# Kernel tuning notes

Hardware: AMD Instinct MI355X
Metric: run time of the kernel (lower is better)

## Reference

```python
import jax, jax.numpy as jnp
import numpy as np

B, S, D, E, H, K = 4, 2048, 1024, 8, 4096, 2


def setup_inputs() -> dict:
    key = jax.random.key(0)
    ks = jax.random.split(key, 6)
    scale_in = 0.02  # keep logits/activations in a sane range
    return {
        "x": jax.random.normal(ks[0], (B, S, D), jnp.float32),
        "gate_w": jax.random.normal(ks[1], (D, E), jnp.float32) * scale_in,
        "noise_weight": jnp.zeros((E,), jnp.float32),  # torch init: zeros
        "noise": jax.random.normal(ks[2], (B, S, E), jnp.float32),
        "w1": jax.random.normal(ks[3], (E, D, H), jnp.float32) * scale_in,
        "b1": jnp.zeros((E, H), jnp.float32),
        "w2": jax.random.normal(ks[4], (E, D, H), jnp.float32) * scale_in,
        "b2": jnp.zeros((E, H), jnp.float32),
        "wp": jax.random.normal(ks[5], (E, H, D), jnp.float32) * scale_in,
        "bp": jnp.zeros((E, D), jnp.float32),
    }


def _moe(x, gate_w, noise_weight, noise, w1, b1, w2, b2, wp, bp):
    b, s, d = x.shape
    # --- noisy top-k gate ---
    logits = jnp.einsum("bsd,de->bse", x, gate_w)          # [B,S,E]
    logits_noisy = logits + noise * noise_weight            # noisy_std = 1.0
    top_v, top_i = jax.lax.top_k(logits_noisy, K)           # [B,S,K]
    # softmax over sparse logits (-inf elsewhere) == softmax over the top-k values
    probs_k = jax.nn.softmax(top_v, axis=-1)                # [B,S,K]
    onehot = jax.nn.one_hot(top_i, E, dtype=x.dtype)        # [B,S,K,E]
    gated = jnp.einsum("bsk,bske->bse", probs_k, onehot)    # [B,S,E]

    # --- dispatch / expert SwiGLU / weighted combine ---
    xf = x.reshape(b * s, d)                                # [T,D]
    gf = gated.reshape(b * s, E).T                          # [E,T]

    def body(acc, p):
        w1e, b1e, w2e, b2e, wpe, bpe, ge = p
        h = (xf @ w1e + b1e) * jax.nn.silu(xf @ w2e + b2e)  # [T,H] SwiGLU
        out = h @ wpe + bpe                                 # [T,D]
        return acc + ge[:, None] * out, None

    acc, _ = jax.lax.scan(body, jnp.zeros_like(xf), (w1, b1, w2, b2, wp, bp, gf))
    return acc.reshape(b, s, d)


def reference(x, gate_w, noise_weight, noise, w1, b1, w2, b2, wp, bp):
    return _moe(x, gate_w, noise_weight, noise, w1, b1, w2, b2, wp, bp)
```

## Files before the change

### kernel.cpp

```cpp
#include <hip/hip_runtime.h>


#define T_TOK 8192
#define DDIM 1024
#define EEXP 8
#define HDIM 4096
#define RMAX 18432

typedef short short8 __attribute__((ext_vector_type(8)));
typedef float f32x4 __attribute__((ext_vector_type(4)));
typedef unsigned short ushort4v __attribute__((ext_vector_type(4)));
typedef unsigned int u32;

__device__ __forceinline__ unsigned short f2bf(float f) {
  unsigned u = __builtin_bit_cast(unsigned, f);
  return (unsigned short)((u + 0x7FFFu + ((u >> 16) & 1u)) >> 16);
}
__device__ __forceinline__ float bf2f(unsigned short b) {
  unsigned u = ((unsigned)b) << 16;
  return __builtin_bit_cast(float, u);
}
__device__ __forceinline__ void gl_lds16(const void* g, void* l) {
  __builtin_amdgcn_global_load_lds((const u32 __attribute__((address_space(1)))*)g,
                                   (u32 __attribute__((address_space(3)))*)l, 16, 0, 0);
}

__global__ void k_convert_w(const float* __restrict__ src, unsigned short* __restrict__ dst,
                            int N, int K) {
  __shared__ float lbuf[64 * 129];
  int e = blockIdx.z, ct = blockIdx.x, kt = blockIdx.y;
  int tid = threadIdx.x;
  const float* s = src + (size_t)e * K * N + (size_t)(kt * 64) * N + ct * 128;
#pragma unroll
  for (int q = 0; q < 8; q++) {
    int idx = q * 256 + tid;
    int row = idx >> 5, c4 = (idx & 31) * 4;
    float4 v = *(const float4*)(s + (size_t)row * N + c4);
    lbuf[row * 129 + c4 + 0] = v.x;
    lbuf[row * 129 + c4 + 1] = v.y;
    lbuf[row * 129 + c4 + 2] = v.z;
    lbuf[row * 129 + c4 + 3] = v.w;
  }
  __syncthreads();
  unsigned short* dt = dst + ((size_t)(e * (N / 128) + ct) * (K / 64) + kt) * 8192;
#pragma unroll
  for (int q = 0; q < 4; q++) {
    int idx = q * 256 + tid;
    int kc = idx & 7, n = idx >> 3;
    short8 o;
#pragma unroll
    for (int j = 0; j < 8; j++) o[j] = (short)f2bf(lbuf[(kc * 8 + j) * 129 + n]);
    int byte = (n * 128 + kc * 16) ^ ((n & 7) << 4);
    *(short8*)((char*)dt + byte) = o;
  }
}

__global__ void k_init(int* __restrict__ rowtok, int* __restrict__ counts, int* __restrict__ cursor) {
  int i = blockIdx.x * 256 + threadIdx.x;
  if (i < RMAX) rowtok[i] = 0;
  if (i < EEXP) { counts[i] = 0; cursor[i] = 0; }
}

__launch_bounds__(256)
__global__ void k_gate(const float* __restrict__ x, const float* __restrict__ gw,
                       const float* __restrict__ nwt, const float* __restrict__ noi,
                       int* __restrict__ tki, float* __restrict__ tkp,
                       int* __restrict__ counts, unsigned short* __restrict__ xb) {
  __shared__ float gwT[8][1024];
  int tid = threadIdx.x;
#pragma unroll
  for (int q = 0; q < 32; q++) {
    int flat = q * 256 + tid;
    gwT[flat & 7][flat >> 3] = gw[flat];
  }
  __syncthreads();
  int wave = tid >> 6, l = tid & 63;
  int t = blockIdx.x * 4 + wave;
  float acc[8] = {0.f, 0.f, 0.f, 0.f, 0.f, 0.f, 0.f, 0.f};
  const float4* xr = (const float4*)(x + (size_t)t * DDIM);
#pragma unroll
  for (int i = 0; i < 4; i++) {
    float4 xv = xr[l + i * 64];
    int d0 = (l + i * 64) * 4;
    ushort4v o;
    o.x = f2bf(xv.x); o.y = f2bf(xv.y); o.z = f2bf(xv.z); o.w = f2bf(xv.w);
    *(ushort4v*)(xb + (size_t)t * DDIM + d0) = o;
#pragma unroll
    for (int e = 0; e < 8; e++) {
      float4 gv = *(const float4*)&gwT[e][d0];
      acc[e] += xv.x * gv.x + xv.y * gv.y + xv.z * gv.z + xv.w * gv.w;
    }
  }
#pragma unroll
  for (int s = 1; s < 64; s <<= 1) {
#pragma unroll
    for (int e = 0; e < 8; e++) acc[e] += __shfl_xor(acc[e], s, 64);
  }
  if (l == 0) {
    float nl[8];
#pragma unroll
    for (int e = 0; e < 8; e++) nl[e] = acc[e] + noi[t * 8 + e] * nwt[e];
    int i0 = 0; float v0 = nl[0];
#pragma unroll
    for (int e = 1; e < 8; e++) if (nl[e] > v0) { v0 = nl[e]; i0 = e; }
    int i1 = -1; float v1 = -3.4e38f;
#pragma unroll
    for (int e = 0; e < 8; e++) if (e != i0 && nl[e] > v1) { v1 = nl[e]; i1 = e; }
    float ex = __expf(v1 - v0);
    float p0 = 1.f / (1.f + ex);
    float p1 = ex * p0;
    tki[2 * t] = i0; tki[2 * t + 1] = i1;
    tkp[2 * t] = p0; tkp[2 * t + 1] = p1;
    atomicAdd(&counts[i0], 1);
    atomicAdd(&counts[i1], 1);
  }
}

__global__ void k_prefix(const int* __restrict__ counts, int* __restrict__ basep) {
  if (threadIdx.x == 0) {
    int b = 0;
    for (int e = 0; e < EEXP; e++) { basep[e] = b; b += (counts[e] + 255) & ~255; }
  }
}

__global__ void k_scatter(const int* __restrict__ tki, const int* __restrict__ basep,
                          int* __restrict__ cursor, int* __restrict__ rowtok,
                          int* __restrict__ t2r) {
  int t = blockIdx.x * 256 + threadIdx.x;
  if (t >= T_TOK) return;
#pragma unroll
  for (int k = 0; k < 2; k++) {
    int e = tki[2 * t + k];
    int pos = atomicAdd(&cursor[e], 1);
    int row = basep[e] + pos;
    rowtok[row] = t;
    t2r[2 * t + k] = row;
  }
}

__launch_bounds__(512, 2)
__global__ void k_gemm1(const unsigned short* __restrict__ xb,
                        const unsigned short* __restrict__ w1s, const unsigned short* __restrict__ w2s,
                        const float* __restrict__ b1g, const float* __restrict__ b2g,
                        const int* __restrict__ counts, const int* __restrict__ basep,
                        const int* __restrict__ rowtok,
                        unsigned short* __restrict__ hout) {
  int e = blockIdx.y >> 6;
  int rt = blockIdx.y & 63;
  int cnt = counts[e];
  if (rt >= ((cnt + 255) >> 8)) return;
  int ct = blockIdx.x;
  int row0 = basep[e] + rt * 256;
  int col0 = ct * 128;

  __shared__ char smem[131072];
  __shared__ int s_tok[256];
  __shared__ float s_b1[128], s_b2[128];

  int tid = threadIdx.x;
  if (tid < 256) s_tok[tid] = rowtok[row0 + tid];
  if (tid < 128) {
    s_b1[tid] = b1g[e * HDIM + col0 + tid];
    s_b2[tid] = b2g[e * HDIM + col0 + tid];
  }
  __syncthreads();

  int wave = tid >> 6, l = tid & 63;
  int wm = wave >> 2, wn = wave & 3;
  int g = l >> 4, ln = l & 15;

  size_t a_src[4]; int a_dst[4];
#pragma unroll
  for (int q = 0; q < 4; q++) {
    int c = q * 512 + tid;
    int r = c >> 3, cc = (c & 7) ^ (r & 7);
    a_src[q] = (size_t)s_tok[r] * (DDIM * 2) + cc * 16;
    a_dst[q] = c * 16;
  }

  f32x4 zero = {0.f, 0.f, 0.f, 0.f};
  f32x4 acc_a[8][2], acc_b[8][2];
#pragma unroll
  for (int m = 0; m < 8; m++)
#pragma unroll
    for (int n = 0; n < 2; n++) { acc_a[m][n] = zero; acc_b[m][n] = zero; }

  const char* xbb = (const char*)xb;
  const char* w1t = (const char*)(w1s + ((size_t)(e * 32 + ct) * 16) * 8192);
  const char* w2t = (const char*)(w2s + ((size_t)(e * 32 + ct) * 16) * 8192);

#define STAGE1(buf, kt)                                                          \
  {                                                                              \
    int _kt = (kt);                                                              \
    _Pragma("unroll") for (int q = 0; q < 4; q++)                                \
      gl_lds16(xbb + a_src[q] + _kt * 128, smem + (buf) * 32768 + a_dst[q]);     \
    _Pragma("unroll") for (int q = 0; q < 2; q++) {                              \
      int c = q * 512 + tid;                                                     \
      gl_lds16(w1t + (size_t)_kt * 16384 + c * 16, smem + 65536 + (buf) * 16384 + c * 16); \
      gl_lds16(w2t + (size_t)_kt * 16384 + c * 16, smem + 98304 + (buf) * 16384 + c * 16); \
    }                                                                            \
  }

  STAGE1(0, 0);
  __syncthreads();

  int cur = 0;
  for (int kt = 0; kt < 16; kt++) {
    if (kt < 15) STAGE1(cur ^ 1, kt + 1);
#pragma unroll
    for (int ks = 0; ks < 2; ks++) {
      int kb = ks * 64 + g * 16;
      short8 af[8], bf1[2], bf2[2];
#pragma unroll
      for (int m = 0; m < 8; m++) {
        int r = wm * 128 + m * 16 + ln;
        af[m] = *(const short8*)(smem + cur * 32768 + ((r * 128 + kb) ^ ((r & 7) << 4)));
      }
#pragma unroll
      for (int n = 0; n < 2; n++) {
        int r = wn * 32 + n * 16 + ln;
        int byte = (r * 128 + kb) ^ ((r & 7) << 4);
        bf1[n] = *(const short8*)(smem + 65536 + cur * 16384 + byte);
        bf2[n] = *(const short8*)(smem + 98304 + cur * 16384 + byte);
      }
#pragma unroll
      for (int m = 0; m < 8; m++)
#pragma unroll
        for (int n = 0; n < 2; n++) {
          acc_a[m][n] = __builtin_amdgcn_mfma_f32_16x16x32_bf16(af[m], bf1[n], acc_a[m][n], 0, 0, 0);
          acc_b[m][n] = __builtin_amdgcn_mfma_f32_16x16x32_bf16(af[m], bf2[n], acc_b[m][n], 0, 0, 0);
        }
    }
    __syncthreads();
    cur ^= 1;
  }

  unsigned short* ht = (unsigned short*)smem;
#pragma unroll
  for (int m = 0; m < 8; m++)
#pragma unroll
    for (int n = 0; n < 2; n++)
#pragma unroll
      for (int r = 0; r < 4; r++) {
        int row = wm * 128 + m * 16 + g * 4 + r;
        int col = wn * 32 + n * 16 + ln;
        float a = acc_a[m][n][r] + s_b1[col];
        float b = acc_b[m][n][r] + s_b2[col];
        float hv = a * (b / (1.f + __expf(-b)));
        ht[row * 128 + col] = f2bf(hv);
      }
  __syncthreads();
#pragma unroll
  for (int q = 0; q < 8; q++) {
    int idx = q * 512 + tid;
    int row = idx >> 4, cc = (idx & 15) * 8;
    short8 v = *(const short8*)(smem + idx * 16);
    *(short8*)(hout + (size_t)(row0 + row) * HDIM + col0 + cc) = v;
  }
}

__launch_bounds__(512, 2)
__global__ void k_gemm2(const unsigned short* __restrict__ hin,
                        const unsigned short* __restrict__ wps, const float* __restrict__ bpg,
                        const int* __restrict__ counts, const int* __restrict__ basep,
                        unsigned short* __restrict__ yout) {
  int e = blockIdx.y >> 6;
  int rt = blockIdx.y & 63;
  int cnt = counts[e];
  if (rt >= ((cnt + 127) >> 7)) return;
  int ct = blockIdx.x;
  int row0 = basep[e] + rt * 128;
  int col0 = ct * 256;

  __shared__ char smem[98304];
  __shared__ float s_bp[256];
  int tid = threadIdx.x;
  if (tid < 256) s_bp[tid] = bpg[e * DDIM + col0 + tid];
  __syncthreads();

  int wave = tid >> 6, l = tid & 63;
  int wm = wave >> 2, wn = wave & 3;
  int g = l >> 4, ln = l & 15;

  size_t a_src[2]; int a_dst[2];
#pragma unroll
  for (int q = 0; q < 2; q++) {
    int c = q * 512 + tid;
    int r = c >> 3, cc = (c & 7) ^ (r & 7);
    a_src[q] = (size_t)(row0 + r) * (HDIM * 2) + cc * 16;
    a_dst[q] = c * 16;
  }

  f32x4 zero = {0.f, 0.f, 0.f, 0.f};
  f32x4 acc[4][4];
#pragma unroll
  for (int m = 0; m < 4; m++)
#pragma unroll
    for (int n = 0; n < 4; n++) acc[m][n] = zero;

  const char* hb = (const char*)hin;
  const char* wpt = (const char*)(wps + ((size_t)(e * 8 + ct * 2) * 64) * 8192);

#define STAGE2(buf, kt)                                                          \
  {                                                                              \
    int _kt = (kt);                                                              \
    _Pragma("unroll") for (int q = 0; q < 2; q++)                                \
      gl_lds16(hb + a_src[q] + _kt * 128, smem + (buf) * 16384 + a_dst[q]);      \
    _Pragma("unroll") for (int q = 0; q < 4; q++) {                              \
      int c = q * 512 + tid;                                                     \
      int sub = c >> 10;                                                         \
      gl_lds16(wpt + (size_t)(sub * 64 + _kt) * 16384 + (c & 1023) * 16,         \
               smem + 32768 + (buf) * 32768 + c * 16);                           \
    }                                                                            \
  }

  STAGE2(0, 0);
  __syncthreads();

  int cur = 0;
  for (int kt = 0; kt < 64; kt++) {
    if (kt < 63) STAGE2(cur ^ 1, kt + 1);
#pragma unroll
    for (int ks = 0; ks < 2; ks++) {
      int kb = ks * 64 + g * 16;
      short8 af[4], bf[4];
#pragma unroll
      for (int m = 0; m < 4; m++) {
        int r = wm * 64 + m * 16 + ln;
        af[m] = *(const short8*)(smem + cur * 16384 + ((r * 128 + kb) ^ ((r & 7) << 4)));
      }
#pragma unroll
      for (int n = 0; n < 4; n++) {
        int rg = wn * 64 + n * 16 + ln;
        int sub = rg >> 7, rr = rg & 127;
        bf[n] = *(const short8*)(smem + 32768 + cur * 32768 + sub * 16384 +
                                 ((rr * 128 + kb) ^ ((rr & 7) << 4)));
      }
#pragma unroll
      for (int m = 0; m < 4; m++)
#pragma unroll
        for (int n = 0; n < 4; n++)
          acc[m][n] = __builtin_amdgcn_mfma_f32_16x16x32_bf16(af[m], bf[n], acc[m][n], 0, 0, 0);
    }
    __syncthreads();
    cur ^= 1;
  }

  unsigned short* ht = (unsigned short*)smem;
#pragma unroll
  for (int m = 0; m < 4; m++)
#pragma unroll
    for (int n = 0; n < 4; n++)
#pragma unroll
      for (int r = 0; r < 4; r++) {
        int row = wm * 64 + m * 16 + g * 4 + r;
        int col = wn * 64 + n * 16 + ln;
        ht[row * 256 + col] = f2bf(acc[m][n][r] + s_bp[col]);
      }
  __syncthreads();
#pragma unroll
  for (int q = 0; q < 8; q++) {
    int idx = q * 512 + tid;
    int row = idx >> 5, cc = (idx & 31) * 8;
    short8 v = *(const short8*)(smem + idx * 16);
    *(short8*)(yout + (size_t)(row0 + row) * DDIM + col0 + cc) = v;
  }
}

__global__ void k_combine(const unsigned short* __restrict__ yv,
                          const int* __restrict__ t2r, const float* __restrict__ tkp,
                          float* __restrict__ outp) {
  int gid = blockIdx.x * 256 + threadIdx.x;
  int t = gid >> 8;
  int c4 = (gid & 255) << 2;
  int r0 = t2r[2 * t], r1 = t2r[2 * t + 1];
  float p0 = tkp[2 * t], p1 = tkp[2 * t + 1];
  ushort4v u0 = *(const ushort4v*)(yv + (size_t)r0 * DDIM + c4);
  ushort4v u1 = *(const ushort4v*)(yv + (size_t)r1 * DDIM + c4);
  float4 o;
  o.x = p0 * bf2f(u0.x) + p1 * bf2f(u1.x);
  o.y = p0 * bf2f(u0.y) + p1 * bf2f(u1.y);
  o.z = p0 * bf2f(u0.z) + p1 * bf2f(u1.z);
  o.w = p0 * bf2f(u0.w) + p1 * bf2f(u1.w);
  *(float4*)(outp + (size_t)t * DDIM + c4) = o;
}

extern "C" void kernel_launch(void* const* d_in, const int* in_sizes, int n_in,
                              void* d_out, int out_size, void* d_ws, size_t ws_size,
                              hipStream_t stream) {
  const float* x   = (const float*)d_in[0];
  const float* gw  = (const float*)d_in[1];
  const float* nwt = (const float*)d_in[2];
  const float* noi = (const float*)d_in[3];
  const float* w1  = (const float*)d_in[4];
  const float* b1  = (const float*)d_in[5];
  const float* w2  = (const float*)d_in[6];
  const float* b2  = (const float*)d_in[7];
  const float* wp  = (const float*)d_in[8];
  const float* bp  = (const float*)d_in[9];
  float* outp = (float*)d_out;
  char* ws = (char*)d_ws;

  constexpr size_t SZ_W = (size_t)EEXP * DDIM * HDIM * 2;
  constexpr size_t OFF_XB  = 0;
  constexpr size_t OFF_W1S = OFF_XB + (size_t)T_TOK * DDIM * 2;
  constexpr size_t OFF_W2S = OFF_W1S + SZ_W;
  constexpr size_t OFF_WPS = OFF_W2S + SZ_W;
  constexpr size_t OFF_H   = OFF_WPS + SZ_W;
  constexpr size_t OFF_Y   = OFF_H + (size_t)RMAX * HDIM * 2;
  constexpr size_t OFF_RT  = OFF_Y + (size_t)RMAX * DDIM * 2;
  constexpr size_t OFF_TKI = OFF_RT + (size_t)RMAX * 4;
  constexpr size_t OFF_TKP = OFF_TKI + (size_t)T_TOK * 2 * 4;
  constexpr size_t OFF_T2R = OFF_TKP + (size_t)T_TOK * 2 * 4;
  constexpr size_t OFF_CNT = OFF_T2R + (size_t)T_TOK * 2 * 4;
  constexpr size_t OFF_BAS = OFF_CNT + 256;
  constexpr size_t OFF_CUR = OFF_BAS + 256;

  unsigned short* xb  = (unsigned short*)(ws + OFF_XB);
  unsigned short* w1s = (unsigned short*)(ws + OFF_W1S);
  unsigned short* w2s = (unsigned short*)(ws + OFF_W2S);
  unsigned short* wps = (unsigned short*)(ws + OFF_WPS);
  unsigned short* h   = (unsigned short*)(ws + OFF_H);
  unsigned short* y   = (unsigned short*)(ws + OFF_Y);
  int*   rowtok = (int*)(ws + OFF_RT);
  int*   tki    = (int*)(ws + OFF_TKI);
  float* tkp    = (float*)(ws + OFF_TKP);
  int*   t2r    = (int*)(ws + OFF_T2R);
  int*   counts = (int*)(ws + OFF_CNT);
  int*   basep  = (int*)(ws + OFF_BAS);
  int*   cursor = (int*)(ws + OFF_CUR);

  dim3 blk(256);
  k_init<<<dim3((RMAX + 255) / 256), blk, 0, stream>>>(rowtok, counts, cursor);
  k_gate<<<dim3(T_TOK / 4), blk, 0, stream>>>(x, gw, nwt, noi, tki, tkp, counts, xb);
  k_convert_w<<<dim3(HDIM / 128, DDIM / 64, EEXP), blk, 0, stream>>>(w1, w1s, HDIM, DDIM);
  k_convert_w<<<dim3(HDIM / 128, DDIM / 64, EEXP), blk, 0, stream>>>(w2, w2s, HDIM, DDIM);
  k_convert_w<<<dim3(DDIM / 128, HDIM / 64, EEXP), blk, 0, stream>>>(wp, wps, DDIM, HDIM);
  k_prefix<<<dim3(1), dim3(64), 0, stream>>>(counts, basep);
  k_scatter<<<dim3(T_TOK / 256), blk, 0, stream>>>(tki, basep, cursor, rowtok, t2r);
  k_gemm1<<<dim3(HDIM / 128, EEXP * 64), dim3(512), 0, stream>>>(xb, w1s, w2s, b1, b2, counts, basep, rowtok, h);
  k_gemm2<<<dim3(DDIM / 256, EEXP * 64), dim3(512), 0, stream>>>(h, wps, bp, counts, basep, y);
  k_combine<<<dim3(T_TOK), blk, 0, stream>>>(y, t2r, tkp, outp);
  (void)in_sizes; (void)n_in; (void)out_size; (void)ws_size;
}
```

Before: 1.081 ms.

## Deepen GEMM pipelines to 4-stage K=32 slots with split barriers and priority

```diff
diff --git a/kernel.cpp b/kernel.cpp
--- a/kernel.cpp
+++ b/kernel.cpp
@@ -24,34 +24,38 @@
   __builtin_amdgcn_global_load_lds((const u32 __attribute__((address_space(1)))*)g,
                                    (u32 __attribute__((address_space(3)))*)l, 16, 0, 0);
 }
+#define BAR() asm volatile("s_barrier" ::: "memory")
+__device__ __forceinline__ void vwait_c(int n) {
+  if (n == 8) asm volatile("s_waitcnt vmcnt(8)" ::: "memory");
+  else if (n == 4) asm volatile("s_waitcnt vmcnt(4)" ::: "memory");
+  else if (n == 0) asm volatile("s_waitcnt vmcnt(0)" ::: "memory");
+}
+#define MFMA_BF16 __builtin_amdgcn_mfma_f32_16x16x32_bf16
 
 __global__ void k_convert_w(const float* __restrict__ src, unsigned short* __restrict__ dst,
                             int N, int K) {
-  __shared__ float lbuf[64 * 129];
+  __shared__ float lbuf[32][130];
   int e = blockIdx.z, ct = blockIdx.x, kt = blockIdx.y;
   int tid = threadIdx.x;
-  const float* s = src + (size_t)e * K * N + (size_t)(kt * 64) * N + ct * 128;
-#pragma unroll
-  for (int q = 0; q < 8; q++) {
+  const float* s = src + (size_t)e * K * N + (size_t)(kt * 32) * N + ct * 128;
+#pragma unroll
+  for (int q = 0; q < 4; q++) {
     int idx = q * 256 + tid;
     int row = idx >> 5, c4 = (idx & 31) * 4;
     float4 v = *(const float4*)(s + (size_t)row * N + c4);
-    lbuf[row * 129 + c4 + 0] = v.x;
-    lbuf[row * 129 + c4 + 1] = v.y;
-    lbuf[row * 129 + c4 + 2] = v.z;
-    lbuf[row * 129 + c4 + 3] = v.w;
-  }
-  __syncthreads();
-  unsigned short* dt = dst + ((size_t)(e * (N / 128) + ct) * (K / 64) + kt) * 8192;
-#pragma unroll
-  for (int q = 0; q < 4; q++) {
+    lbuf[row][c4 + 0] = v.x; lbuf[row][c4 + 1] = v.y;
+    lbuf[row][c4 + 2] = v.z; lbuf[row][c4 + 3] = v.w;
+  }
+  __syncthreads();
+  char* dt = (char*)dst + ((size_t)(e * (N / 128) + ct) * (K / 32) + kt) * 8192;
+#pragma unroll
+  for (int q = 0; q < 2; q++) {
     int idx = q * 256 + tid;
-    int kc = idx & 7, n = idx >> 3;
+    int n = idx >> 2, kc = idx & 3;
     short8 o;
 #pragma unroll
-    for (int j = 0; j < 8; j++) o[j] = (short)f2bf(lbuf[(kc * 8 + j) * 129 + n]);
-    int byte = (n * 128 + kc * 16) ^ ((n & 7) << 4);
-    *(short8*)((char*)dt + byte) = o;
+    for (int j = 0; j < 8; j++) o[j] = (short)f2bf(lbuf[kc * 8 + j][n]);
+    *(short8*)(dt + ((n * 64 + kc * 16) ^ ((n & 3) << 4))) = o;
   }
 }
 
@@ -169,13 +173,23 @@
   int wm = wave >> 2, wn = wave & 3;
   int g = l >> 4, ln = l & 15;
 
-  size_t a_src[4]; int a_dst[4];
-#pragma unroll
-  for (int q = 0; q < 4; q++) {
-    int c = q * 512 + tid;
-    int r = c >> 3, cc = (c & 7) ^ (r & 7);
-    a_src[q] = (size_t)s_tok[r] * (DDIM * 2) + cc * 16;
-    a_dst[q] = c * 16;
+  int c0 = tid, c1 = 512 + tid;
+  int r0s = c0 >> 2, k0s = c0 & 3, r1s = c1 >> 2, k1s = c1 & 3;
+  size_t a_src0 = (size_t)s_tok[r0s] * 2048 + (size_t)((k0s ^ (r0s & 3)) * 16);
+  size_t a_src1 = (size_t)s_tok[r1s] * 2048 + (size_t)((k1s ^ (r1s & 3)) * 16);
+  int a_dst0 = c0 * 16, a_dst1 = c1 * 16;
+
+  int a_rd[8];
+#pragma unroll
+  for (int m = 0; m < 8; m++) {
+    int r = wm * 128 + m * 16 + ln;
+    a_rd[m] = r * 64 + ((g * 16) ^ ((r & 3) << 4));
+  }
+  int b_rd[2];
+#pragma unroll
+  for (int n = 0; n < 2; n++) {
+    int r = wn * 32 + n * 16 + ln;
+    b_rd[n] = r * 64 + ((g * 16) ^ ((r & 3) << 4));
   }
 
   f32x4 zero = {0.f, 0.f, 0.f, 0.f};
@@ -186,55 +200,59 @@
     for (int n = 0; n < 2; n++) { acc_a[m][n] = zero; acc_b[m][n] = zero; }
 
   const char* xbb = (const char*)xb;
-  const char* w1t = (const char*)(w1s + ((size_t)(e * 32 + ct) * 16) * 8192);
-  const char* w2t = (const char*)(w2s + ((size_t)(e * 32 + ct) * 16) * 8192);
-
-#define STAGE1(buf, kt)                                                          \
-  {                                                                              \
-    int _kt = (kt);                                                              \
-    _Pragma("unroll") for (int q = 0; q < 4; q++)                                \
-      gl_lds16(xbb + a_src[q] + _kt * 128, smem + (buf) * 32768 + a_dst[q]);     \
-    _Pragma("unroll") for (int q = 0; q < 2; q++) {                              \
-      int c = q * 512 + tid;                                                     \
-      gl_lds16(w1t + (size_t)_kt * 16384 + c * 16, smem + 65536 + (buf) * 16384 + c * 16); \
-      gl_lds16(w2t + (size_t)_kt * 16384 + c * 16, smem + 98304 + (buf) * 16384 + c * 16); \
-    }                                                                            \
-  }
-
-  STAGE1(0, 0);
-  __syncthreads();
-
-  int cur = 0;
-  for (int kt = 0; kt < 16; kt++) {
-    if (kt < 15) STAGE1(cur ^ 1, kt + 1);
-#pragma unroll
-    for (int ks = 0; ks < 2; ks++) {
-      int kb = ks * 64 + g * 16;
-      short8 af[8], bf1[2], bf2[2];
-#pragma unroll
-      for (int m = 0; m < 8; m++) {
-        int r = wm * 128 + m * 16 + ln;
-        af[m] = *(const short8*)(smem + cur * 32768 + ((r * 128 + kb) ^ ((r & 7) << 4)));
-      }
-#pragma unroll
-      for (int n = 0; n < 2; n++) {
-        int r = wn * 32 + n * 16 + ln;
-        int byte = (r * 128 + kb) ^ ((r & 7) << 4);
-        bf1[n] = *(const short8*)(smem + 65536 + cur * 16384 + byte);
-        bf2[n] = *(const short8*)(smem + 98304 + cur * 16384 + byte);
-      }
-#pragma unroll
-      for (int m = 0; m < 8; m++)
-#pragma unroll
-        for (int n = 0; n < 2; n++) {
-          acc_a[m][n] = __builtin_amdgcn_mfma_f32_16x16x32_bf16(af[m], bf1[n], acc_a[m][n], 0, 0, 0);
-          acc_b[m][n] = __builtin_amdgcn_mfma_f32_16x16x32_bf16(af[m], bf2[n], acc_b[m][n], 0, 0, 0);
-        }
-    }
-    __syncthreads();
-    cur ^= 1;
-  }
-
+  const char* w1t = (const char*)w1s + (size_t)(e * 32 + ct) * 32 * 8192;
+  const char* w2t = (const char*)w2s + (size_t)(e * 32 + ct) * 32 * 8192;
+
+#define G1_PRE(s) { int nb = (s) & 3;                                            \
+    gl_lds16(xbb + a_src0 + (size_t)(s) * 64, smem + nb * 16384 + a_dst0);       \
+    gl_lds16(xbb + a_src1 + (size_t)(s) * 64, smem + nb * 16384 + a_dst1);       \
+    gl_lds16(w1t + (size_t)(s) * 8192 + tid * 16, smem + 65536 + nb * 8192 + tid * 16); \
+    gl_lds16(w2t + (size_t)(s) * 8192 + tid * 16, smem + 98304 + nb * 8192 + tid * 16); }
+
+  G1_PRE(0) G1_PRE(1) G1_PRE(2)
+  vwait_c(8); BAR();
+
+#define G1_SLOT(s, ISSUE, VMN) {                                                 \
+    int bs = (s) & 3;                                                            \
+    char* Ab = smem + bs * 16384;                                                \
+    char* B1b = smem + 65536 + bs * 8192;                                        \
+    char* B2b = smem + 98304 + bs * 8192;                                        \
+    short8 af[4], b1f[2], b2f[2];                                                \
+    _Pragma("unroll") for (int m = 0; m < 4; m++) af[m] = *(const short8*)(Ab + a_rd[m]); \
+    b1f[0] = *(const short8*)(B1b + b_rd[0]); b1f[1] = *(const short8*)(B1b + b_rd[1]); \
+    b2f[0] = *(const short8*)(B2b + b_rd[0]); b2f[1] = *(const short8*)(B2b + b_rd[1]); \
+    if (ISSUE) { int ns = (s) + 3, nb = ns & 3;                                  \
+      gl_lds16(xbb + a_src0 + (size_t)ns * 64, smem + nb * 16384 + a_dst0);      \
+      gl_lds16(xbb + a_src1 + (size_t)ns * 64, smem + nb * 16384 + a_dst1); }    \
+    BAR();                                                                       \
+    __builtin_amdgcn_s_setprio(1);                                               \
+    _Pragma("unroll") for (int m = 0; m < 4; m++) {                              \
+      acc_a[m][0] = MFMA_BF16(af[m], b1f[0], acc_a[m][0], 0, 0, 0);              \
+      acc_a[m][1] = MFMA_BF16(af[m], b1f[1], acc_a[m][1], 0, 0, 0);              \
+      acc_b[m][0] = MFMA_BF16(af[m], b2f[0], acc_b[m][0], 0, 0, 0);              \
+      acc_b[m][1] = MFMA_BF16(af[m], b2f[1], acc_b[m][1], 0, 0, 0); }            \
+    __builtin_amdgcn_s_setprio(0);                                               \
+    BAR();                                                                       \
+    _Pragma("unroll") for (int m = 0; m < 4; m++) af[m] = *(const short8*)(Ab + a_rd[4 + m]); \
+    if (ISSUE) { int ns = (s) + 3, nb = ns & 3;                                  \
+      gl_lds16(w1t + (size_t)ns * 8192 + tid * 16, smem + 65536 + nb * 8192 + tid * 16); \
+      gl_lds16(w2t + (size_t)ns * 8192 + tid * 16, smem + 98304 + nb * 8192 + tid * 16); } \
+    BAR();                                                                       \
+    __builtin_amdgcn_s_setprio(1);                                               \
+    _Pragma("unroll") for (int m = 0; m < 4; m++) {                              \
+      acc_a[4 + m][0] = MFMA_BF16(af[m], b1f[0], acc_a[4 + m][0], 0, 0, 0);      \
+      acc_a[4 + m][1] = MFMA_BF16(af[m], b1f[1], acc_a[4 + m][1], 0, 0, 0);      \
+      acc_b[4 + m][0] = MFMA_BF16(af[m], b2f[0], acc_b[4 + m][0], 0, 0, 0);      \
+      acc_b[4 + m][1] = MFMA_BF16(af[m], b2f[1], acc_b[4 + m][1], 0, 0, 0); }    \
+    __builtin_amdgcn_s_setprio(0);                                               \
+    vwait_c(VMN); BAR(); }
+
+  for (int s = 0; s < 29; ++s) { G1_SLOT(s, 1, 8) }
+  G1_SLOT(29, 0, 4)
+  G1_SLOT(30, 0, 0)
+  G1_SLOT(31, 0, -1)
+
+  __syncthreads();
   unsigned short* ht = (unsigned short*)smem;
 #pragma unroll
   for (int m = 0; m < 8; m++)
@@ -267,12 +285,12 @@
   int e = blockIdx.y >> 6;
   int rt = blockIdx.y & 63;
   int cnt = counts[e];
-  if (rt >= ((cnt + 127) >> 7)) return;
+  if (rt >= ((cnt + 255) >> 8)) return;
   int ct = blockIdx.x;
-  int row0 = basep[e] + rt * 128;
+  int row0 = basep[e] + rt * 256;
   int col0 = ct * 256;
 
-  __shared__ char smem[98304];
+  __shared__ char smem[131072];
   __shared__ float s_bp[256];
   int tid = threadIdx.x;
   if (tid < 256) s_bp[tid] = bpg[e * DDIM + col0 + tid];
@@ -282,84 +300,95 @@
   int wm = wave >> 2, wn = wave & 3;
   int g = l >> 4, ln = l & 15;
 
-  size_t a_src[2]; int a_dst[2];
-#pragma unroll
-  for (int q = 0; q < 2; q++) {
-    int c = q * 512 + tid;
-    int r = c >> 3, cc = (c & 7) ^ (r & 7);
-    a_src[q] = (size_t)(row0 + r) * (HDIM * 2) + cc * 16;
-    a_dst[q] = c * 16;
+  int c0 = tid, c1 = 512 + tid;
+  int r0s = c0 >> 2, k0s = c0 & 3, r1s = c1 >> 2, k1s = c1 & 3;
+  size_t a_src0 = (size_t)(row0 + r0s) * 8192 + (size_t)((k0s ^ (r0s & 3)) * 16);
+  size_t a_src1 = (size_t)(row0 + r1s) * 8192 + (size_t)((k1s ^ (r1s & 3)) * 16);
+  int a_dst0 = c0 * 16, a_dst1 = c1 * 16;
+  const char* b_src0 = (const char*)wps + (size_t)(e * 8 + ct * 2 + 0) * 128 * 8192 + (size_t)(c0 & 511) * 16;
+  const char* b_src1 = (const char*)wps + (size_t)(e * 8 + ct * 2 + 1) * 128 * 8192 + (size_t)(c1 & 511) * 16;
+
+  int a_rd[8];
+#pragma unroll
+  for (int m = 0; m < 8; m++) {
+    int r = wm * 128 + m * 16 + ln;
+    a_rd[m] = r * 64 + ((g * 16) ^ ((r & 3) << 4));
+  }
+  int b_rd[4];
+#pragma unroll
+  for (int n = 0; n < 4; n++) {
+    int ncol = wn * 64 + n * 16 + ln;
+    int sub = ncol >> 7, r = ncol & 127;
+    b_rd[n] = sub * 8192 + r * 64 + ((g * 16) ^ ((r & 3) << 4));
   }
 
   f32x4 zero = {0.f, 0.f, 0.f, 0.f};
-  f32x4 acc[4][4];
-#pragma unroll
-  for (int m = 0; m < 4; m++)
+  f32x4 acc[8][4];
+#pragma unroll
+  for (int m = 0; m < 8; m++)
 #pragma unroll
     for (int n = 0; n < 4; n++) acc[m][n] = zero;
 
   const char* hb = (const char*)hin;
-  const char* wpt = (const char*)(wps + ((size_t)(e * 8 + ct * 2) * 64) * 8192);
-
-#define STAGE2(buf, kt)                                                          \
-  {                                                                              \
-    int _kt = (kt);                                                              \
-    _Pragma("unroll") for (int q = 0; q < 2; q++)                                \
-      gl_lds16(hb + a_src[q] + _kt * 128, smem + (buf) * 16384 + a_dst[q]);      \
-    _Pragma("unroll") for (int q = 0; q < 4; q++) {                              \
-      int c = q * 512 + tid;                                                     \
-      int sub = c >> 10;                                                         \
-      gl_lds16(wpt + (size_t)(sub * 64 + _kt) * 16384 + (c & 1023) * 16,         \
-               smem + 32768 + (buf) * 32768 + c * 16);                           \
-    }                                                                            \
-  }
-
-  STAGE2(0, 0);
-  __syncthreads();
-
-  int cur = 0;
-  for (int kt = 0; kt < 64; kt++) {
-    if (kt < 63) STAGE2(cur ^ 1, kt + 1);
-#pragma unroll
-    for (int ks = 0; ks < 2; ks++) {
-      int kb = ks * 64 + g * 16;
-      short8 af[4], bf[4];
-#pragma unroll
-      for (int m = 0; m < 4; m++) {
-        int r = wm * 64 + m * 16 + ln;
-        af[m] = *(const short8*)(smem + cur * 16384 + ((r * 128 + kb) ^ ((r & 7) << 4)));
-      }
-#pragma unroll
-      for (int n = 0; n < 4; n++) {
-        int rg = wn * 64 + n * 16 + ln;
-        int sub = rg >> 7, rr = rg & 127;
-        bf[n] = *(const short8*)(smem + 32768 + cur * 32768 + sub * 16384 +
-                                 ((rr * 128 + kb) ^ ((rr & 7) << 4)));
-      }
-#pragma unroll
-      for (int m = 0; m < 4; m++)
-#pragma unroll
-        for (int n = 0; n < 4; n++)
-          acc[m][n] = __builtin_amdgcn_mfma_f32_16x16x32_bf16(af[m], bf[n], acc[m][n], 0, 0, 0);
-    }
-    __syncthreads();
-    cur ^= 1;
-  }
-
+
+#define G2_PRE(s) { int nb = (s) & 3;                                            \
+    gl_lds16(hb + a_src0 + (size_t)(s) * 64, smem + nb * 16384 + a_dst0);        \
+    gl_lds16(hb + a_src1 + (size_t)(s) * 64, smem + nb * 16384 + a_dst1);        \
+    gl_lds16(b_src0 + (size_t)(s) * 8192, smem + 65536 + nb * 16384 + a_dst0);   \
+    gl_lds16(b_src1 + (size_t)(s) * 8192, smem + 65536 + nb * 16384 + a_dst1); }
+
+  G2_PRE(0) G2_PRE(1) G2_PRE(2)
+  vwait_c(8); BAR();
+
+#define G2_SLOT(s, ISSUE, VMN) {                                                 \
+    int bs = (s) & 3;                                                            \
+    char* Ab = smem + bs * 16384;                                                \
+    char* Bb = smem + 65536 + bs * 16384;                                        \
+    short8 af[4], bf[4];                                                         \
+    _Pragma("unroll") for (int m = 0; m < 4; m++) af[m] = *(const short8*)(Ab + a_rd[m]); \
+    _Pragma("unroll") for (int n = 0; n < 4; n++) bf[n] = *(const short8*)(Bb + b_rd[n]); \
+    if (ISSUE) { int ns = (s) + 3, nb = ns & 3;                                  \
+      gl_lds16(hb + a_src0 + (size_t)ns * 64, smem + nb * 16384 + a_dst0);       \
+      gl_lds16(hb + a_src1 + (size_t)ns * 64, smem + nb * 16384 + a_dst1); }     \
+    BAR();                                                                       \
+    __builtin_amdgcn_s_setprio(1);                                               \
+    _Pragma("unroll") for (int m = 0; m < 4; m++)                                \
+      _Pragma("unroll") for (int n = 0; n < 4; n++)                              \
+        acc[m][n] = MFMA_BF16(af[m], bf[n], acc[m][n], 0, 0, 0);                 \
+    __builtin_amdgcn_s_setprio(0);                                               \
+    BAR();                                                                       \
+    _Pragma("unroll") for (int m = 0; m < 4; m++) af[m] = *(const short8*)(Ab + a_rd[4 + m]); \
+    if (ISSUE) { int ns = (s) + 3, nb = ns & 3;                                  \
+      gl_lds16(b_src0 + (size_t)ns * 8192, smem + 65536 + nb * 16384 + a_dst0);  \
+      gl_lds16(b_src1 + (size_t)ns * 8192, smem + 65536 + nb * 16384 + a_dst1); }\
+    BAR();                                                                       \
+    __builtin_amdgcn_s_setprio(1);                                               \
+    _Pragma("unroll") for (int m = 0; m < 4; m++)                                \
+      _Pragma("unroll") for (int n = 0; n < 4; n++)                              \
+        acc[4 + m][n] = MFMA_BF16(af[m], bf[n], acc[4 + m][n], 0, 0, 0);         \
+    __builtin_amdgcn_s_setprio(0);                                               \
+    vwait_c(VMN); BAR(); }
+
+  for (int s = 0; s < 125; ++s) { G2_SLOT(s, 1, 8) }
+  G2_SLOT(125, 0, 4)
+  G2_SLOT(126, 0, 0)
+  G2_SLOT(127, 0, -1)
+
+  __syncthreads();
   unsigned short* ht = (unsigned short*)smem;
 #pragma unroll
-  for (int m = 0; m < 4; m++)
+  for (int m = 0; m < 8; m++)
 #pragma unroll
     for (int n = 0; n < 4; n++)
 #pragma unroll
       for (int r = 0; r < 4; r++) {
-        int row = wm * 64 + m * 16 + g * 4 + r;
+        int row = wm * 128 + m * 16 + g * 4 + r;
         int col = wn * 64 + n * 16 + ln;
         ht[row * 256 + col] = f2bf(acc[m][n][r] + s_bp[col]);
       }
   __syncthreads();
 #pragma unroll
-  for (int q = 0; q < 8; q++) {
+  for (int q = 0; q < 16; q++) {
     int idx = q * 512 + tid;
     int row = idx >> 5, cc = (idx & 31) * 8;
     short8 v = *(const short8*)(smem + idx * 16);
@@ -433,9 +462,9 @@
   dim3 blk(256);
   k_init<<<dim3((RMAX + 255) / 256), blk, 0, stream>>>(rowtok, counts, cursor);
   k_gate<<<dim3(T_TOK / 4), blk, 0, stream>>>(x, gw, nwt, noi, tki, tkp, counts, xb);
-  k_convert_w<<<dim3(HDIM / 128, DDIM / 64, EEXP), blk, 0, stream>>>(w1, w1s, HDIM, DDIM);
-  k_convert_w<<<dim3(HDIM / 128, DDIM / 64, EEXP), blk, 0, stream>>>(w2, w2s, HDIM, DDIM);
-  k_convert_w<<<dim3(DDIM / 128, HDIM / 64, EEXP), blk, 0, stream>>>(wp, wps, DDIM, HDIM);
+  k_convert_w<<<dim3(HDIM / 128, DDIM / 32, EEXP), blk, 0, stream>>>(w1, w1s, HDIM, DDIM);
+  k_convert_w<<<dim3(HDIM / 128, DDIM / 32, EEXP), blk, 0, stream>>>(w2, w2s, HDIM, DDIM);
+  k_convert_w<<<dim3(DDIM / 128, HDIM / 32, EEXP), blk, 0, stream>>>(wp, wps, DDIM, HDIM);
   k_prefix<<<dim3(1), dim3(64), 0, stream>>>(counts, basep);
   k_scatter<<<dim3(T_TOK / 256), blk, 0, stream>>>(tki, basep, cursor, rowtok, t2r);
   k_gemm1<<<dim3(HDIM / 128, EEXP * 64), dim3(512), 0, stream>>>(xb, w1s, w2s, b1, b2, counts, basep, rowtok, h);
```

New measurement: 1.041 ms. -3.7%, faster.
